# Kernel optimization log

Measured on AMD Instinct MI355X. Metric: run time of the kernel, lower is better.

Reference implementation:

```python
import jax, jax.numpy as jnp
import numpy as np

DIM = 1024
HEADS = 16
HEAD_DIM = DIM // HEADS

def setup_inputs() -> dict:
    key = jax.random.key(0)
    ks = jax.random.split(key, 6)
    s = 0.02
    return {
        "x": jax.random.normal(ks[0], (2, 2048, DIM), dtype=jnp.float32),
        "w_qkv": jax.random.normal(ks[1], (DIM, 3 * DIM), dtype=jnp.float32) * s,
        "w_proj": jax.random.normal(ks[2], (DIM, DIM), dtype=jnp.float32) * s,
        "b_proj": jnp.zeros((DIM,), dtype=jnp.float32),
        "ln_gamma": jnp.ones((DIM,), dtype=jnp.float32),
        "ln_beta": jnp.zeros((DIM,), dtype=jnp.float32),
    }

def layer_norm(x, gamma, beta, eps=1e-5):
    mu = jnp.mean(x, axis=-1, keepdims=True)
    var = jnp.var(x, axis=-1, keepdims=True)
    return (x - mu) * jax.lax.rsqrt(var + eps) * gamma + beta

def reference(x, w_qkv, w_proj, b_proj, ln_gamma, ln_beta):
    B, N, C = x.shape
    residual = x
    h = layer_norm(x, ln_gamma, ln_beta)
    qkv = h @ w_qkv  # [B,N,3C]
    qkv = qkv.reshape(B, N, 3, HEADS, HEAD_DIM)
    q = jnp.transpose(qkv[:, :, 0], (0, 2, 1, 3))  # [B,H,N,D]
    k = jnp.transpose(qkv[:, :, 1], (0, 2, 1, 3))
    v = jnp.transpose(qkv[:, :, 2], (0, 2, 1, 3))
    scale = 1.0 / jnp.sqrt(jnp.float32(HEAD_DIM))
    attn = jnp.einsum('bhqd,bhkd->bhqk', q, k) * scale
    attn = jax.nn.softmax(attn, axis=-1)
    out = jnp.einsum('bhqk,bhkd->bhqd', attn, v)  # [B,H,N,D]
    out = jnp.transpose(out, (0, 2, 1, 3)).reshape(B, N, C)
    out = out @ w_proj + b_proj
    return out + residual
```

## Files before the change

### kernel.cpp

```cpp
#include <hip/hip_runtime.h>

#define DIM   1024
#define HEADS 16
#define HDIM  64
#define BATCH 2
#define SEQ   2048
#define TOK   (BATCH*SEQ)
#define MEG   1048576

typedef __bf16 bf16x8 __attribute__((ext_vector_type(8)));
typedef float  f32x4  __attribute__((ext_vector_type(4)));
typedef float  f32x16 __attribute__((ext_vector_type(16)));

__device__ __forceinline__ float b2f(ushort u) {
    union { unsigned int u32; float f; } x; x.u32 = ((unsigned int)u) << 16; return x.f;
}
__device__ __forceinline__ ushort f2b(float f) {
    union { float f; unsigned int u32; } x; x.f = f;
    unsigned int r = x.u32 + 0x7FFFu + ((x.u32 >> 16) & 1u);
    return (ushort)(r >> 16);
}
__device__ __forceinline__ void gload_lds16(const ushort* g, void* l) {
    __builtin_amdgcn_global_load_lds((const __attribute__((address_space(1))) void*)g,
                                     (__attribute__((address_space(3))) void*)l, 16, 0, 0);
}
__device__ __forceinline__ float fexp2(float x) {
    float r; asm("v_exp_f32 %0, %1" : "=v"(r) : "v"(x)); return r;
}
__device__ __forceinline__ unsigned int cvtpk_bf16(float lo, float hi) {
    unsigned int r; asm("v_cvt_pk_bf16_f32 %0, %1, %2" : "=v"(r) : "v"(lo), "v"(hi)); return r;
}
__device__ __forceinline__ void plane32swap(unsigned int &a, unsigned int &b) {
    asm("v_permlane32_swap_b32 %0, %1" : "+v"(a), "+v"(b));
}
__device__ __forceinline__ bf16x8 pack8(float e0, float e1, float e2, float e3,
                                        float e4, float e5, float e6, float e7) {
    unsigned int a = cvtpk_bf16(e0, e1), b = cvtpk_bf16(e2, e3);
    unsigned int c = cvtpk_bf16(e4, e5), d = cvtpk_bf16(e6, e7);
    plane32swap(a, c); plane32swap(b, d);
    union { unsigned int u[4]; bf16x8 v; } r;
    r.u[0] = a; r.u[1] = b; r.u[2] = c; r.u[3] = d;
    return r.v;
}

__global__ void transpose_f2b_k(const float* __restrict__ src, ushort* __restrict__ dst,
                                int R, int Cc) {
    __shared__ ushort tile[32][33];
    int c0 = blockIdx.x * 32, r0 = blockIdx.y * 32;
    int tx = threadIdx.x, ty = threadIdx.y;
#pragma unroll
    for (int i = 0; i < 4; i++)
        tile[ty + 8 * i][tx] = f2b(src[(long)(r0 + ty + 8 * i) * Cc + c0 + tx]);
    __syncthreads();
#pragma unroll
    for (int i = 0; i < 4; i++)
        dst[(long)(c0 + ty + 8 * i) * R + r0 + tx] = tile[tx][ty + 8 * i];
}

__global__ __launch_bounds__(256)
void ln_k(const float* __restrict__ x, const float* __restrict__ gamma,
          const float* __restrict__ beta, ushort* __restrict__ h) {
    __shared__ float red[8];
    int row = blockIdx.x, tid = threadIdx.x;
    const float* xr = x + (long)row * DIM;
    float4 xv = *(const float4*)(xr + tid * 4);
    float s1 = xv.x + xv.y + xv.z + xv.w;
    float s2 = xv.x * xv.x + xv.y * xv.y + xv.z * xv.z + xv.w * xv.w;
#pragma unroll
    for (int off = 32; off; off >>= 1) {
        s1 += __shfl_down(s1, off);
        s2 += __shfl_down(s2, off);
    }
    int wid = tid >> 6, lane = tid & 63;
    if (lane == 0) { red[wid * 2] = s1; red[wid * 2 + 1] = s2; }
    __syncthreads();
    s1 = red[0] + red[2] + red[4] + red[6];
    s2 = red[1] + red[3] + red[5] + red[7];
    float mu  = s1 * (1.0f / DIM);
    float var = s2 * (1.0f / DIM) - mu * mu;
    float rs  = rsqrtf(var + 1e-5f);
    float4 gv = *(const float4*)(gamma + tid * 4);
    float4 bv = *(const float4*)(beta + tid * 4);
    ushort4 ov;
    ov.x = f2b((xv.x - mu) * rs * gv.x + bv.x);
    ov.y = f2b((xv.y - mu) * rs * gv.y + bv.y);
    ov.z = f2b((xv.z - mu) * rs * gv.z + bv.z);
    ov.w = f2b((xv.w - mu) * rs * gv.w + bv.w);
    *(ushort4*)(h + (long)row * DIM + tid * 4) = ov;
}

__global__ __launch_bounds__(256, 3)
void gemm_qkv_k(const ushort* __restrict__ A, const ushort* __restrict__ Bt,
                ushort* __restrict__ qp, ushort* __restrict__ kp, ushort* __restrict__ vp) {
    __shared__ ushort smem[16384];
    int tid  = threadIdx.x;
    int wid  = tid >> 6, lane = tid & 63;
    int quad = lane >> 4, l16 = lane & 15;
    int wm = wid >> 1, wn = wid & 1;
    int rowbase = blockIdx.y * 128;
    int colbase = blockIdx.x * 128;

    f32x4 acc[4][4];
#pragma unroll
    for (int i = 0; i < 4; i++)
#pragma unroll
        for (int j = 0; j < 4; j++) acc[i][j] = (f32x4){0.f, 0.f, 0.f, 0.f};

    for (int k0 = 0; k0 < DIM; k0 += 64) {
#pragma unroll
        for (int p = 0; p < 2; p++) {
            int c = wid * 2 + p;
            int r = c * 16 + (lane >> 2);
            int ac = (lane & 3) * 8;
#pragma unroll
            for (int pnl = 0; pnl < 2; pnl++) {
                int cc = k0 + pnl * 32 + ac;
                gload_lds16(A  + (long)(rowbase + r) * DIM + cc,
                            &smem[pnl * 4096 + c * 16 * 32]);
                gload_lds16(Bt + (long)(colbase + r) * DIM + cc,
                            &smem[8192 + pnl * 4096 + c * 16 * 32]);
            }
        }
        __syncthreads();
#pragma unroll
        for (int pnl = 0; pnl < 2; pnl++) {
            bf16x8 fa[4], fb[4];
#pragma unroll
            for (int t = 0; t < 4; t++)
                fa[t] = *(const bf16x8*)(&smem[pnl * 4096 + (wm * 64 + t * 16 + l16) * 32 + quad * 8]);
#pragma unroll
            for (int t = 0; t < 4; t++)
                fb[t] = *(const bf16x8*)(&smem[8192 + pnl * 4096 + (wn * 64 + t * 16 + l16) * 32 + quad * 8]);
#pragma unroll
            for (int i = 0; i < 4; i++)
#pragma unroll
                for (int j = 0; j < 4; j++)
                    acc[i][j] = __builtin_amdgcn_mfma_f32_16x16x32_bf16(fa[i], fb[j], acc[i][j], 0, 0, 0);
        }
        __syncthreads();
    }

    if (colbase >= 2048) {
#pragma unroll
        for (int i = 0; i < 4; i++)
#pragma unroll
            for (int j = 0; j < 4; j++) {
                int cl = wn * 64 + j * 16 + l16;
                int rl = wm * 64 + i * 16 + quad * 4;
#pragma unroll
                for (int r = 0; r < 4; r++)
                    smem[cl * 128 + rl + r] = f2b(acc[i][j][r]);
            }
        __syncthreads();
        int b = rowbase >> 11, nnb = rowbase & 2047;
        int hbase = (colbase - 2048) >> 6;
#pragma unroll
        for (int i = 0; i < 8; i++) {
            int id = i * 256 + tid;
            int cl = id >> 4;
            int off = (id & 15) * 8;
            int hh = hbase + (cl >> 6), d = cl & 63;
            uint4 val = *(const uint4*)(&smem[cl * 128 + off]);
            *(uint4*)(vp + (((long)b * HEADS + hh) * HDIM + d) * SEQ + nnb + off) = val;
        }
    } else {
#pragma unroll
        for (int i = 0; i < 4; i++)
#pragma unroll
            for (int j = 0; j < 4; j++) {
                int m0  = rowbase + wm * 64 + i * 16 + quad * 4;
                int col = colbase + wn * 64 + j * 16 + l16;
                int part = col >> 10, rem = col & 1023;
                int head = rem >> 6, d = rem & 63;
                ushort* dst = (part == 0) ? qp : kp;
#pragma unroll
                for (int r = 0; r < 4; r++) {
                    float v = acc[i][j][r];
                    int mm = m0 + r;
                    int b = mm >> 11, nn = mm & 2047;
                    float sv = (part == 0) ? v * 0.18033688011f : v;
                    dst[((((long)b * HEADS + head) * SEQ + nn) << 6) + d] = f2b(sv);
                }
            }
    }
}

__global__ __launch_bounds__(256, 3)
void gemm_proj_k(const ushort* __restrict__ A, const ushort* __restrict__ Bt,
                 const float* __restrict__ bias, const float* __restrict__ xres,
                 float* __restrict__ outp) {
    __shared__ ushort As[2][128][32];
    __shared__ ushort Bs[2][64][32];
    int tid  = threadIdx.x;
    int wid  = tid >> 6, lane = tid & 63;
    int quad = lane >> 4, l16 = lane & 15;
    int rowbase = blockIdx.y * 128;
    int colbase = blockIdx.x * 64;
    int arow = lane >> 2, acol = (lane & 3) * 8;

    f32x4 acc[2][4];
#pragma unroll
    for (int i = 0; i < 2; i++)
#pragma unroll
        for (int j = 0; j < 4; j++) acc[i][j] = (f32x4){0.f, 0.f, 0.f, 0.f};

    for (int k0 = 0; k0 < DIM; k0 += 64) {
#pragma unroll
        for (int p = 0; p < 2; p++) {
            int c = wid * 2 + p;
            int r = c * 16 + arow;
            int mm = rowbase + r;
            int bq = mm >> 11, nn = mm & 2047;
#pragma unroll
            for (int pnl = 0; pnl < 2; pnl++) {
                int cc = k0 + pnl * 32 + acol;
                int head = cc >> 6, d = cc & 63;
                gload_lds16(A + ((((long)bq * HEADS + head) * SEQ + nn) << 6) + d,
                            &As[pnl][c * 16][0]);
            }
        }
        {
            int r = wid * 16 + arow;
#pragma unroll
            for (int pnl = 0; pnl < 2; pnl++) {
                int cc = k0 + pnl * 32 + acol;
                gload_lds16(Bt + (long)(colbase + r) * DIM + cc, &Bs[pnl][wid * 16][0]);
            }
        }
        __syncthreads();
#pragma unroll
        for (int pnl = 0; pnl < 2; pnl++) {
            bf16x8 fa[2], fb[4];
#pragma unroll
            for (int t = 0; t < 2; t++)
                fa[t] = *(const bf16x8*)(&As[pnl][wid * 32 + t * 16 + l16][quad * 8]);
#pragma unroll
            for (int t = 0; t < 4; t++)
                fb[t] = *(const bf16x8*)(&Bs[pnl][t * 16 + l16][quad * 8]);
#pragma unroll
            for (int i = 0; i < 2; i++)
#pragma unroll
                for (int j = 0; j < 4; j++)
                    acc[i][j] = __builtin_amdgcn_mfma_f32_16x16x32_bf16(fa[i], fb[j], acc[i][j], 0, 0, 0);
        }
        __syncthreads();
    }

#pragma unroll
    for (int i = 0; i < 2; i++)
#pragma unroll
        for (int j = 0; j < 4; j++) {
            int m0  = rowbase + wid * 32 + i * 16 + quad * 4;
            int col = colbase + j * 16 + l16;
#pragma unroll
            for (int r = 0; r < 4; r++) {
                int mm = m0 + r;
                outp[(long)mm * DIM + col] = acc[i][j][r] + bias[col] + xres[(long)mm * DIM + col];
            }
        }
}

__global__ __launch_bounds__(256, 2)
void attn_k(ushort* qio, const ushort* __restrict__ kg,
            const ushort* __restrict__ vt) {
    __shared__ __align__(16) ushort Kp[2][4096];
    __shared__ __align__(16) ushort Vs[2][4096];
    int bh = blockIdx.y;
    int tid = threadIdx.x, wid = tid >> 6;
    int lane = tid & 63;
    int l31 = lane & 31, hi = lane >> 5;
    ushort* qh = qio + (long)bh * SEQ * HDIM;
    const ushort* kh = kg + (long)bh * SEQ * HDIM;
    const ushort* vh = vt + (long)bh * HDIM * SEQ;

    int srow = tid >> 3, schk = tid & 7;
    int sofs = srow * 64 + ((schk ^ (srow & 7)) * 8);
    const ushort* kbase = kh + (long)srow * HDIM + schk * 8;
    const ushort* vbase = vh + (long)srow * SEQ + schk * 8;

    int qrow0 = blockIdx.x * 128 + wid * 32;
    bf16x8 qf[4];
#pragma unroll
    for (int ks = 0; ks < 4; ks++)
        qf[ks] = *(const bf16x8*)(qh + (long)(qrow0 + l31) * HDIM + ks * 16 + hi * 8);

    f32x16 o0 = {}, o1 = {};
    f32x4 lac = {0.f, 0.f, 0.f, 0.f};

    uint4 kr0 = *(const uint4*)(kbase);
    uint4 kr1 = *(const uint4*)(kbase + 32 * HDIM);
    uint4 vr0 = *(const uint4*)(vbase);
    uint4 vr1 = *(const uint4*)(vbase + 32 * SEQ);
    *(uint4*)(&Kp[0][sofs])        = kr0;
    *(uint4*)(&Kp[0][sofs + 2048]) = kr1;
    *(uint4*)(&Vs[0][sofs])        = vr0;
    *(uint4*)(&Vs[0][sofs + 2048]) = vr1;

    const int NIT = SEQ / 64;
    for (int it = 0; it < NIT; ++it) {
        int buf = it & 1;
        if (it + 1 < NIT) {
            int kt = (it + 1) * 64;
            kr0 = *(const uint4*)(kbase + (long)kt * HDIM);
            kr1 = *(const uint4*)(kbase + (long)(kt + 32) * HDIM);
            vr0 = *(const uint4*)(vbase + kt);
            vr1 = *(const uint4*)(vbase + 32 * SEQ + kt);
        }
        __syncthreads();

        f32x16 sc0 = {}, sc1 = {};
        __builtin_amdgcn_s_setprio(1);
#pragma unroll
        for (int ks = 0; ks < 4; ks++) {
            int psl = ((2 * ks + hi) ^ (l31 & 7)) * 8;
            bf16x8 ka = *(const bf16x8*)(&Kp[buf][l31 * 64 + psl]);
            bf16x8 kb = *(const bf16x8*)(&Kp[buf][(32 + l31) * 64 + psl]);
            sc0 = __builtin_amdgcn_mfma_f32_32x32x16_bf16(ka, qf[ks], sc0, 0, 0, 0);
            sc1 = __builtin_amdgcn_mfma_f32_32x32x16_bf16(kb, qf[ks], sc1, 0, 0, 0);
        }
        __builtin_amdgcn_s_setprio(0);

        float e0[16], e1[16];
#pragma unroll
        for (int r = 0; r < 16; r++) { e0[r] = fexp2(sc0[r]); e1[r] = fexp2(sc1[r]); }
#pragma unroll
        for (int r = 0; r < 4; r++)
            lac += (f32x4){e0[4*r], e0[4*r+1], e0[4*r+2], e0[4*r+3]}
                 + (f32x4){e1[4*r], e1[4*r+1], e1[4*r+2], e1[4*r+3]};

        bf16x8 pa0 = pack8(e0[0], e0[1], e0[2],  e0[3],  e0[4],  e0[5],  e0[6],  e0[7]);
        bf16x8 pa1 = pack8(e0[8], e0[9], e0[10], e0[11], e0[12], e0[13], e0[14], e0[15]);
        bf16x8 pa2 = pack8(e1[0], e1[1], e1[2],  e1[3],  e1[4],  e1[5],  e1[6],  e1[7]);
        bf16x8 pa3 = pack8(e1[8], e1[9], e1[10], e1[11], e1[12], e1[13], e1[14], e1[15]);

        __builtin_amdgcn_s_setprio(1);
#pragma unroll
        for (int g = 0; g < 4; g++) {
            int psl = ((2 * g + hi) ^ (l31 & 7)) * 8;
            bf16x8 v0 = *(const bf16x8*)(&Vs[buf][l31 * 64 + psl]);
            bf16x8 v1 = *(const bf16x8*)(&Vs[buf][(32 + l31) * 64 + psl]);
            bf16x8 pg = (g == 0) ? pa0 : (g == 1) ? pa1 : (g == 2) ? pa2 : pa3;
            o0 = __builtin_amdgcn_mfma_f32_32x32x16_bf16(pg, v0, o0, 0, 0, 0);
            o1 = __builtin_amdgcn_mfma_f32_32x32x16_bf16(pg, v1, o1, 0, 0, 0);
        }
        __builtin_amdgcn_s_setprio(0);

        if (it + 1 < NIT) {
            *(uint4*)(&Kp[buf ^ 1][sofs])        = kr0;
            *(uint4*)(&Kp[buf ^ 1][sofs + 2048]) = kr1;
            *(uint4*)(&Vs[buf ^ 1][sofs])        = vr0;
            *(uint4*)(&Vs[buf ^ 1][sofs + 2048]) = vr1;
        }
    }

    float t = lac[0] + lac[1] + lac[2] + lac[3];
    t += __shfl_xor(t, 32);
    float linv = 1.0f / t;
#pragma unroll
    for (int r = 0; r < 16; r++) {
        int qrow = (r & 3) + 8 * (r >> 2) + 4 * hi;
        float lr = __shfl(linv, qrow);
        long ro = (long)(qrow0 + qrow) * HDIM;
        qh[ro + l31]      = f2b(o0[r] * lr);
        qh[ro + 32 + l31] = f2b(o1[r] * lr);
    }
}

extern "C" void kernel_launch(void* const* d_in, const int* in_sizes, int n_in,
                              void* d_out, int out_size, void* d_ws, size_t ws_size,
                              hipStream_t stream) {
    const float* x      = (const float*)d_in[0];
    const float* w_qkv  = (const float*)d_in[1];
    const float* w_proj = (const float*)d_in[2];
    const float* b_proj = (const float*)d_in[3];
    const float* gamma  = (const float*)d_in[4];
    const float* beta   = (const float*)d_in[5];
    float* out = (float*)d_out;

    ushort* ws   = (ushort*)d_ws;
    ushort* h    = ws;
    ushort* wqt  = ws + (size_t)4 * MEG;
    ushort* qb   = ws + (size_t)7 * MEG;
    ushort* kb   = ws + (size_t)11 * MEG;
    ushort* vtb  = ws + (size_t)15 * MEG;

    transpose_f2b_k<<<dim3(3 * DIM / 32, DIM / 32), dim3(32, 8), 0, stream>>>(
        w_qkv, wqt, DIM, 3 * DIM);
    ln_k<<<dim3(TOK), dim3(256), 0, stream>>>(x, gamma, beta, h);
    gemm_qkv_k<<<dim3(3 * DIM / 128, TOK / 128), dim3(256), 0, stream>>>(
        h, wqt, qb, kb, vtb);
    attn_k<<<dim3(SEQ / 128, BATCH * HEADS), dim3(256), 0, stream>>>(qb, kb, vtb);
    transpose_f2b_k<<<dim3(DIM / 32, DIM / 32), dim3(32, 8), 0, stream>>>(
        w_proj, kb, DIM, DIM);
    gemm_proj_k<<<dim3(DIM / 64, TOK / 128), dim3(256), 0, stream>>>(
        qb, kb, b_proj, x, out);
}
```

Measured before the change: 184.3 us.

## Load K/V fragments directly from global into registers, drop LDS staging

The attention kernel no longer stages K and V tiles through double-buffered shared memory. Each wave loads its MFMA operand fragments directly from global memory into registers, using a two-stage software prefetch that alternates register sets. This removes block-wide barriers and LDS traffic. In exchange, each wave loads the full K/V tile independently, which multiplies global/L2 reads, uses less coalesced access, and raises register pressure that may hurt occupancy.

```diff
diff --git a/kernel.cpp b/kernel.cpp
--- a/kernel.cpp
+++ b/kernel.cpp
@@ -260,24 +260,65 @@
         }
 }
 
+__device__ __forceinline__ void load_kv(const ushort* kb0, const ushort* kb1,
+                                        const ushort* vb0, const ushort* vb1, int kt,
+                                        bf16x8 (&kf)[8], bf16x8 (&vf)[8]) {
+#pragma unroll
+    for (int g = 0; g < 4; g++) {
+        kf[2*g]   = *(const bf16x8*)(kb0 + (long)kt * HDIM + g * 16);
+        kf[2*g+1] = *(const bf16x8*)(kb1 + (long)kt * HDIM + g * 16);
+        vf[2*g]   = *(const bf16x8*)(vb0 + kt + g * 16);
+        vf[2*g+1] = *(const bf16x8*)(vb1 + kt + g * 16);
+    }
+}
+
+__device__ __forceinline__ void attn_body(const bf16x8 (&kf)[8], const bf16x8 (&vf)[8],
+                                          const bf16x8 (&qf)[4],
+                                          f32x16 &o0, f32x16 &o1, f32x4 &lac) {
+    f32x16 sc0 = {}, sc1 = {};
+    __builtin_amdgcn_s_setprio(1);
+#pragma unroll
+    for (int ks = 0; ks < 4; ks++) {
+        sc0 = __builtin_amdgcn_mfma_f32_32x32x16_bf16(kf[2*ks],   qf[ks], sc0, 0, 0, 0);
+        sc1 = __builtin_amdgcn_mfma_f32_32x32x16_bf16(kf[2*ks+1], qf[ks], sc1, 0, 0, 0);
+    }
+    __builtin_amdgcn_s_setprio(0);
+
+    float e0[16], e1[16];
+#pragma unroll
+    for (int r = 0; r < 16; r++) { e0[r] = fexp2(sc0[r]); e1[r] = fexp2(sc1[r]); }
+#pragma unroll
+    for (int r = 0; r < 4; r++)
+        lac += (f32x4){e0[4*r], e0[4*r+1], e0[4*r+2], e0[4*r+3]}
+             + (f32x4){e1[4*r], e1[4*r+1], e1[4*r+2], e1[4*r+3]};
+
+    bf16x8 pa0 = pack8(e0[0], e0[1], e0[2],  e0[3],  e0[4],  e0[5],  e0[6],  e0[7]);
+    bf16x8 pa1 = pack8(e0[8], e0[9], e0[10], e0[11], e0[12], e0[13], e0[14], e0[15]);
+    bf16x8 pa2 = pack8(e1[0], e1[1], e1[2],  e1[3],  e1[4],  e1[5],  e1[6],  e1[7]);
+    bf16x8 pa3 = pack8(e1[8], e1[9], e1[10], e1[11], e1[12], e1[13], e1[14], e1[15]);
+
+    __builtin_amdgcn_s_setprio(1);
+    o0 = __builtin_amdgcn_mfma_f32_32x32x16_bf16(pa0, vf[0], o0, 0, 0, 0);
+    o1 = __builtin_amdgcn_mfma_f32_32x32x16_bf16(pa0, vf[1], o1, 0, 0, 0);
+    o0 = __builtin_amdgcn_mfma_f32_32x32x16_bf16(pa1, vf[2], o0, 0, 0, 0);
+    o1 = __builtin_amdgcn_mfma_f32_32x32x16_bf16(pa1, vf[3], o1, 0, 0, 0);
+    o0 = __builtin_amdgcn_mfma_f32_32x32x16_bf16(pa2, vf[4], o0, 0, 0, 0);
+    o1 = __builtin_amdgcn_mfma_f32_32x32x16_bf16(pa2, vf[5], o1, 0, 0, 0);
+    o0 = __builtin_amdgcn_mfma_f32_32x32x16_bf16(pa3, vf[6], o0, 0, 0, 0);
+    o1 = __builtin_amdgcn_mfma_f32_32x32x16_bf16(pa3, vf[7], o1, 0, 0, 0);
+    __builtin_amdgcn_s_setprio(0);
+}
+
 __global__ __launch_bounds__(256, 2)
 void attn_k(ushort* qio, const ushort* __restrict__ kg,
             const ushort* __restrict__ vt) {
-    __shared__ __align__(16) ushort Kp[2][4096];
-    __shared__ __align__(16) ushort Vs[2][4096];
     int bh = blockIdx.y;
-    int tid = threadIdx.x, wid = tid >> 6;
-    int lane = tid & 63;
+    int tid = threadIdx.x, wid = tid >> 6, lane = tid & 63;
     int l31 = lane & 31, hi = lane >> 5;
     ushort* qh = qio + (long)bh * SEQ * HDIM;
     const ushort* kh = kg + (long)bh * SEQ * HDIM;
     const ushort* vh = vt + (long)bh * HDIM * SEQ;
 
-    int srow = tid >> 3, schk = tid & 7;
-    int sofs = srow * 64 + ((schk ^ (srow & 7)) * 8);
-    const ushort* kbase = kh + (long)srow * HDIM + schk * 8;
-    const ushort* vbase = vh + (long)srow * SEQ + schk * 8;
-
     int qrow0 = blockIdx.x * 128 + wid * 32;
     bf16x8 qf[4];
 #pragma unroll
@@ -287,71 +328,24 @@
     f32x16 o0 = {}, o1 = {};
     f32x4 lac = {0.f, 0.f, 0.f, 0.f};
 
-    uint4 kr0 = *(const uint4*)(kbase);
-    uint4 kr1 = *(const uint4*)(kbase + 32 * HDIM);
-    uint4 vr0 = *(const uint4*)(vbase);
-    uint4 vr1 = *(const uint4*)(vbase + 32 * SEQ);
-    *(uint4*)(&Kp[0][sofs])        = kr0;
-    *(uint4*)(&Kp[0][sofs + 2048]) = kr1;
-    *(uint4*)(&Vs[0][sofs])        = vr0;
-    *(uint4*)(&Vs[0][sofs + 2048]) = vr1;
+    const ushort* kb0 = kh + (long)l31 * HDIM + hi * 8;
+    const ushort* kb1 = kh + (long)(32 + l31) * HDIM + hi * 8;
+    const ushort* vb0 = vh + (long)l31 * SEQ + hi * 8;
+    const ushort* vb1 = vh + (long)(32 + l31) * SEQ + hi * 8;
+
+    bf16x8 ka[8], va[8], kn[8], vn[8];
+    load_kv(kb0, kb1, vb0, vb1, 0, ka, va);
 
     const int NIT = SEQ / 64;
-    for (int it = 0; it < NIT; ++it) {
-        int buf = it & 1;
-        if (it + 1 < NIT) {
-            int kt = (it + 1) * 64;
-            kr0 = *(const uint4*)(kbase + (long)kt * HDIM);
-            kr1 = *(const uint4*)(kbase + (long)(kt + 32) * HDIM);
-            vr0 = *(const uint4*)(vbase + kt);
-            vr1 = *(const uint4*)(vbase + 32 * SEQ + kt);
-        }
-        __syncthreads();
-
-        f32x16 sc0 = {}, sc1 = {};
-        __builtin_amdgcn_s_setprio(1);
-#pragma unroll
-        for (int ks = 0; ks < 4; ks++) {
-            int psl = ((2 * ks + hi) ^ (l31 & 7)) * 8;
-            bf16x8 ka = *(const bf16x8*)(&Kp[buf][l31 * 64 + psl]);
-            bf16x8 kb = *(const bf16x8*)(&Kp[buf][(32 + l31) * 64 + psl]);
-            sc0 = __builtin_amdgcn_mfma_f32_32x32x16_bf16(ka, qf[ks], sc0, 0, 0, 0);
-            sc1 = __builtin_amdgcn_mfma_f32_32x32x16_bf16(kb, qf[ks], sc1, 0, 0, 0);
-        }
-        __builtin_amdgcn_s_setprio(0);
-
-        float e0[16], e1[16];
-#pragma unroll
-        for (int r = 0; r < 16; r++) { e0[r] = fexp2(sc0[r]); e1[r] = fexp2(sc1[r]); }
-#pragma unroll
-        for (int r = 0; r < 4; r++)
-            lac += (f32x4){e0[4*r], e0[4*r+1], e0[4*r+2], e0[4*r+3]}
-                 + (f32x4){e1[4*r], e1[4*r+1], e1[4*r+2], e1[4*r+3]};
-
-        bf16x8 pa0 = pack8(e0[0], e0[1], e0[2],  e0[3],  e0[4],  e0[5],  e0[6],  e0[7]);
-        bf16x8 pa1 = pack8(e0[8], e0[9], e0[10], e0[11], e0[12], e0[13], e0[14], e0[15]);
-        bf16x8 pa2 = pack8(e1[0], e1[1], e1[2],  e1[3],  e1[4],  e1[5],  e1[6],  e1[7]);
-        bf16x8 pa3 = pack8(e1[8], e1[9], e1[10], e1[11], e1[12], e1[13], e1[14], e1[15]);
-
-        __builtin_amdgcn_s_setprio(1);
-#pragma unroll
-        for (int g = 0; g < 4; g++) {
-            int psl = ((2 * g + hi) ^ (l31 & 7)) * 8;
-            bf16x8 v0 = *(const bf16x8*)(&Vs[buf][l31 * 64 + psl]);
-            bf16x8 v1 = *(const bf16x8*)(&Vs[buf][(32 + l31) * 64 + psl]);
-            bf16x8 pg = (g == 0) ? pa0 : (g == 1) ? pa1 : (g == 2) ? pa2 : pa3;
-            o0 = __builtin_amdgcn_mfma_f32_32x32x16_bf16(pg, v0, o0, 0, 0, 0);
-            o1 = __builtin_amdgcn_mfma_f32_32x32x16_bf16(pg, v1, o1, 0, 0, 0);
-        }
-        __builtin_amdgcn_s_setprio(0);
-
-        if (it + 1 < NIT) {
-            *(uint4*)(&Kp[buf ^ 1][sofs])        = kr0;
-            *(uint4*)(&Kp[buf ^ 1][sofs + 2048]) = kr1;
-            *(uint4*)(&Vs[buf ^ 1][sofs])        = vr0;
-            *(uint4*)(&Vs[buf ^ 1][sofs + 2048]) = vr1;
-        }
-    }
+    for (int it = 0; it < NIT - 2; it += 2) {
+        load_kv(kb0, kb1, vb0, vb1, (it + 1) * 64, kn, vn);
+        attn_body(ka, va, qf, o0, o1, lac);
+        load_kv(kb0, kb1, vb0, vb1, (it + 2) * 64, ka, va);
+        attn_body(kn, vn, qf, o0, o1, lac);
+    }
+    load_kv(kb0, kb1, vb0, vb1, (NIT - 1) * 64, kn, vn);
+    attn_body(ka, va, qf, o0, o1, lac);
+    attn_body(kn, vn, qf, o0, o1, lac);
 
     float t = lac[0] + lac[1] + lac[2] + lac[3];
     t += __shfl_xor(t, 32);
```

Measured after the change: 257.2 us. +39.5%, slower.
